# Performance work log

Measured on AMD Instinct MI355X. Metric: run time of the kernel, lower is better.

Reference implementation:

```python
import jax, jax.numpy as jnp
import numpy as np

MU_DT = 0.01
INIT_STD = 0.05

# hidden layers use tanh; last layer is identity (utils.Linear())

def setup_inputs() -> dict:
    key = jax.random.key(0)
    ks = jax.random.split(key, 7)
    B = 512
    nodes = [1024, 4096, 4096, 3072]
    img_batch = jax.random.normal(ks[0], (B, nodes[3]), dtype=jnp.float32)
    mu0 = INIT_STD * jax.random.normal(ks[1], (B, nodes[0]), dtype=jnp.float32)
    mu1 = INIT_STD * jax.random.normal(ks[2], (B, nodes[1]), dtype=jnp.float32)
    mu2 = INIT_STD * jax.random.normal(ks[3], (B, nodes[2]), dtype=jnp.float32)
    W0 = jax.random.normal(ks[4], (nodes[0], nodes[1]), dtype=jnp.float32) / jnp.sqrt(jnp.float32(nodes[0]))
    W1 = jax.random.normal(ks[5], (nodes[1], nodes[2]), dtype=jnp.float32) / jnp.sqrt(jnp.float32(nodes[1]))
    W2 = jax.random.normal(ks[6], (nodes[2], nodes[3]), dtype=jnp.float32) / jnp.sqrt(jnp.float32(nodes[2]))
    return {"img_batch": img_batch, "mu0": mu0, "mu1": mu1, "mu2": mu2,
            "W0": W0, "W1": W1, "W2": W2, "n_iters": 20}


def reference(img_batch, mu0, mu1, mu2, W0, W1, W2, n_iters):
    Ws = (W0, W1, W2)
    L = 3  # n_layers
    acts = (jnp.tanh, jnp.tanh, lambda h: h)
    dacts = (lambda h: 1.0 - jnp.tanh(h) ** 2,
             lambda h: 1.0 - jnp.tanh(h) ** 2,
             lambda h: jnp.ones_like(h))

    def preds_errs(mus):
        # preds[0] = 0, so errs[0] = mus[0]
        hs, errs = [], [mus[0]]
        for l in range(L):
            h = mus[l] @ Ws[l]          # [B, nodes[l+1]]
            hs.append(h)
            errs.append(mus[l + 1] - acts[l](h))
        return hs, errs

    def body(mus, _):
        # prediction pass with current mus (matches stored layer inputs/errs)
        hs, errs = preds_errs(mus)
        new_mus = []
        for l in range(L):
            back = (errs[l + 1] * dacts[l](hs[l])) @ Ws[l].T
            new_mus.append(mus[l] + MU_DT * (back - errs[l]))
        new_mus.append(mus[L])  # target clamped
        return tuple(new_mus), None

    mus = (mu0, mu1, mu2, img_batch)
    mus, _ = jax.lax.scan(body, mus, None, length=n_iters)
    # final prediction/error pass (end of last torch iteration)
    _, errs = preds_errs(mus)
    return jnp.concatenate(errs, axis=1)  # [B, 1024+4096+4096+3072]
```

## Files before the change

### kernel.cpp

```cpp
#include <hip/hip_runtime.h>
#include <hip/hip_bf16.h>
#include <stdint.h>

typedef __hip_bfloat16 bf16_t;
typedef __attribute__((ext_vector_type(8))) short bf16x8;
typedef __attribute__((ext_vector_type(4))) float f32x4;

#define MU_DT 0.01f

__device__ inline void gload_lds16(const void* g, void* lds) {
  __builtin_amdgcn_global_load_lds((const __attribute__((address_space(1))) void*)g,
                                   (__attribute__((address_space(3))) void*)lds, 16, 0, 0);
}

struct GemmLayer {
  const bf16_t* A;
  const bf16_t* Bt;
  const float*  X;
  const float*  E;
  float*        O1;
  bf16_t*       O2;
  int K, N, ostride, mode;
};

struct GemmArgs {
  GemmLayer L[3];
  int start1, start2;
  int tn0, tn1, tn2;
};

__global__ __launch_bounds__(512) void gemm_merged(GemmArgs args) {
  __shared__ __align__(16) bf16_t As[2 * 64 * 64];
  __shared__ __align__(16) bf16_t Bs[2 * 128 * 64];

  const int bid = blockIdx.x;
  int l, local, tilesN;
  if (bid >= args.start2)      { l = 2; local = bid - args.start2; tilesN = args.tn2; }
  else if (bid >= args.start1) { l = 1; local = bid - args.start1; tilesN = args.tn1; }
  else                         { l = 0; local = bid;               tilesN = args.tn0; }
  const GemmLayer Lr = args.L[l];
  const int tm = local / tilesN;
  const int tn = local % tilesN;
  const int K = Lr.K;
  const int rowBase = tm * 64;
  const int colBase = tn * 128;

  const int tid  = threadIdx.x;
  const int lane = tid & 63;
  const int wv   = tid >> 6;
  const int wrM  = wv >> 2;
  const int wcN  = wv & 3;
  const int lo   = lane & 15, hi = lane >> 4;

  f32x4 acc[2][2];
#pragma unroll
  for (int m = 0; m < 2; ++m)
#pragma unroll
    for (int n = 0; n < 2; ++n)
      acc[m][n] = f32x4{0.f, 0.f, 0.f, 0.f};

  char* AsB = (char*)As;
  char* BsB = (char*)Bs;

  const bf16_t* pA0;
  const bf16_t* pB[2];
  {
    const int c = tid;
    const int r = c >> 3, sw = (c & 7) ^ (r & 7);
    pA0 = Lr.A + (size_t)(rowBase + r) * K + sw * 8;
  }
#pragma unroll
  for (int j = 0; j < 2; ++j) {
    const int c = j * 512 + tid;
    const int r = c >> 3, sw = (c & 7) ^ (r & 7);
    pB[j] = Lr.Bt + (size_t)(colBase + r) * K + sw * 8;
  }

  int aoff[2][2], boff[2][2];
#pragma unroll
  for (int m = 0; m < 2; ++m) {
    const int row = wrM * 32 + m * 16 + lo;
#pragma unroll
    for (int kk = 0; kk < 2; ++kk)
      aoff[m][kk] = row * 128 + (((kk * 4 + hi) ^ (row & 7)) << 4);
  }
#pragma unroll
  for (int n = 0; n < 2; ++n) {
    const int row = wcN * 32 + n * 16 + lo;
#pragma unroll
    for (int kk = 0; kk < 2; ++kk)
      boff[n][kk] = row * 128 + (((kk * 4 + hi) ^ (row & 7)) << 4);
  }

  const int waveB = wv * 1024;
  const int nkt = K >> 6;

  gload_lds16(pA0,   AsB + waveB);
  gload_lds16(pB[0], BsB + waveB);
  gload_lds16(pB[1], BsB + 8192 + waveB);
  __syncthreads();

  int cur = 0;
  for (int kt = 0; kt < nkt; ++kt) {
    const int curA = cur * 8192, curB = cur * 16384;
    if (kt + 1 < nkt) {
      const int ke = (kt + 1) * 64;
      gload_lds16(pA0 + ke,   AsB + (curA ^ 8192) + waveB);
      gload_lds16(pB[0] + ke, BsB + (curB ^ 16384) + waveB);
      gload_lds16(pB[1] + ke, BsB + (curB ^ 16384) + 8192 + waveB);
    }

    bf16x8 a[2][2], b[2][2];
#pragma unroll
    for (int m = 0; m < 2; ++m)
#pragma unroll
      for (int kk = 0; kk < 2; ++kk)
        a[m][kk] = *(const bf16x8*)(AsB + curA + aoff[m][kk]);
#pragma unroll
    for (int n = 0; n < 2; ++n)
#pragma unroll
      for (int kk = 0; kk < 2; ++kk)
        b[n][kk] = *(const bf16x8*)(BsB + curB + boff[n][kk]);

#pragma unroll
    for (int kk = 0; kk < 2; ++kk)
#pragma unroll
      for (int m = 0; m < 2; ++m)
#pragma unroll
        for (int n = 0; n < 2; ++n)
          acc[m][n] = __builtin_amdgcn_mfma_f32_16x16x32_bf16(a[m][kk], b[n][kk], acc[m][n], 0, 0, 0);

    if (kt + 1 < nkt) {
      __syncthreads();
      cur ^= 1;
    }
  }

  const int N = Lr.N;
#pragma unroll
  for (int m = 0; m < 2; ++m) {
#pragma unroll
    for (int n = 0; n < 2; ++n) {
#pragma unroll
      for (int r = 0; r < 4; ++r) {
        const int row = rowBase + wrM * 32 + m * 16 + hi * 4 + r;
        const int col = colBase + wcN * 32 + n * 16 + lo;
        const float v = acc[m][n][r];
        const size_t iN = (size_t)row * N + col;
        const size_t iO = (size_t)row * Lr.ostride + col;
        if (Lr.mode == 0) {
          const float mu = Lr.X[iN];
          const float t  = tanhf(v);
          const float e  = mu - t;
          Lr.O1[iO] = e;
          Lr.O2[iN] = __float2bfloat16(e * (1.0f - t * t));
        } else if (Lr.mode == 1) {
          const float e = Lr.X[iN] - v;
          Lr.O1[iO] = e;
          Lr.O2[iN] = __float2bfloat16(e);
        } else if (Lr.mode == 2) {
          const float mu = Lr.X[iN];
          const float nv = mu + MU_DT * (v - mu);
          Lr.O1[iN] = nv;
          Lr.O2[iN] = __float2bfloat16(nv);
        } else {
          const float mu = Lr.X[iN];
          const float e  = Lr.E[iN];
          const float nv = mu + MU_DT * (v - e);
          Lr.O1[iN] = nv;
          Lr.O2[iN] = __float2bfloat16(nv);
        }
      }
    }
  }
}

__global__ void prep_weight(const float* __restrict__ W, bf16_t* __restrict__ Wb,
                            bf16_t* __restrict__ WTb, int R, int C) {
  __shared__ bf16_t t[64][65];
  const int tx = threadIdx.x, ty = threadIdx.y;
  const int c0 = blockIdx.x * 64, r0 = blockIdx.y * 64;
  for (int rr = ty; rr < 64; rr += 4) {
    const float v = W[(size_t)(r0 + rr) * C + c0 + tx];
    const bf16_t b = __float2bfloat16(v);
    Wb[(size_t)(r0 + rr) * C + c0 + tx] = b;
    t[rr][tx] = b;
  }
  __syncthreads();
  for (int rr = ty; rr < 64; rr += 4) {
    WTb[(size_t)(c0 + rr) * R + r0 + tx] = t[tx][rr];
  }
}

__global__ void copy_cast(const float* __restrict__ in, float* __restrict__ of,
                          bf16_t* __restrict__ ob, int n) {
  const int i = blockIdx.x * blockDim.x + threadIdx.x;
  if (i < n) {
    const float v = in[i];
    of[i] = v;
    ob[i] = __float2bfloat16(v);
  }
}

__global__ void copy_e0(const float* __restrict__ mu0, float* __restrict__ out) {
  const int i = blockIdx.x * blockDim.x + threadIdx.x;
  if (i < 512 * 1024) {
    const int b = i >> 10, j = i & 1023;
    out[(size_t)b * 12288 + j] = mu0[i];
  }
}

extern "C" void kernel_launch(void* const* d_in, const int* in_sizes, int n_in,
                              void* d_out, int out_size, void* d_ws, size_t ws_size,
                              hipStream_t stream) {
  const float* img  = (const float*)d_in[0];
  const float* mu0i = (const float*)d_in[1];
  const float* mu1i = (const float*)d_in[2];
  const float* mu2i = (const float*)d_in[3];
  const float* W0   = (const float*)d_in[4];
  const float* W1   = (const float*)d_in[5];
  const float* W2   = (const float*)d_in[6];
  float* out = (float*)d_out;
  const int n_iters = 20;

  char* p = (char*)d_ws;
  auto alloc = [&](size_t bytes) -> char* {
    char* r = p;
    p += (bytes + 255) & ~(size_t)255;
    return r;
  };
  bf16_t* Wb0 = (bf16_t*)alloc((size_t)1024 * 4096 * 2);
  bf16_t* Wb1 = (bf16_t*)alloc((size_t)4096 * 4096 * 2);
  bf16_t* Wb2 = (bf16_t*)alloc((size_t)4096 * 3072 * 2);
  bf16_t* WT0 = (bf16_t*)alloc((size_t)4096 * 1024 * 2);
  bf16_t* WT1 = (bf16_t*)alloc((size_t)4096 * 4096 * 2);
  bf16_t* WT2 = (bf16_t*)alloc((size_t)3072 * 4096 * 2);
  float*  mu0 = (float*)alloc((size_t)512 * 1024 * 4);
  float*  mu1 = (float*)alloc((size_t)512 * 4096 * 4);
  float*  mu2 = (float*)alloc((size_t)512 * 4096 * 4);
  bf16_t* mb0 = (bf16_t*)alloc((size_t)512 * 1024 * 2);
  bf16_t* mb1 = (bf16_t*)alloc((size_t)512 * 4096 * 2);
  bf16_t* mb2 = (bf16_t*)alloc((size_t)512 * 4096 * 2);
  float*  e1  = (float*)alloc((size_t)512 * 4096 * 4);
  float*  e2  = (float*)alloc((size_t)512 * 4096 * 4);
  float*  e3  = (float*)alloc((size_t)512 * 3072 * 4);
  bf16_t* G0  = (bf16_t*)alloc((size_t)512 * 4096 * 2);
  bf16_t* G1  = (bf16_t*)alloc((size_t)512 * 4096 * 2);
  bf16_t* G2  = (bf16_t*)alloc((size_t)512 * 3072 * 2);
  (void)ws_size;

  dim3 tb(64, 4);
  prep_weight<<<dim3(4096 / 64, 1024 / 64), tb, 0, stream>>>(W0, Wb0, WT0, 1024, 4096);
  prep_weight<<<dim3(4096 / 64, 4096 / 64), tb, 0, stream>>>(W1, Wb1, WT1, 4096, 4096);
  prep_weight<<<dim3(3072 / 64, 4096 / 64), tb, 0, stream>>>(W2, Wb2, WT2, 4096, 3072);
  copy_cast<<<(512 * 1024 + 255) / 256, 256, 0, stream>>>(mu0i, mu0, mb0, 512 * 1024);
  copy_cast<<<(512 * 4096 + 255) / 256, 256, 0, stream>>>(mu1i, mu1, mb1, 512 * 4096);
  copy_cast<<<(512 * 4096 + 255) / 256, 256, 0, stream>>>(mu2i, mu2, mb2, 512 * 4096);

  GemmArgs fa;
  fa.L[0] = { mb0, WT0, mu1, nullptr, e1, G0, 1024, 4096, 4096, 0 };
  fa.L[1] = { mb1, WT1, mu2, nullptr, e2, G1, 4096, 4096, 4096, 0 };
  fa.L[2] = { mb2, WT2, img, nullptr, e3, G2, 4096, 3072, 3072, 1 };
  fa.tn0 = 32; fa.tn1 = 32; fa.tn2 = 24;
  fa.start1 = 8 * 32;
  fa.start2 = fa.start1 + 8 * 32;
  const int fwdBlocks = fa.start2 + 8 * 24;

  GemmArgs faF = fa;
  faF.L[0].O1 = out + 1024; faF.L[0].ostride = 12288;
  faF.L[1].O1 = out + 5120; faF.L[1].ostride = 12288;
  faF.L[2].O1 = out + 9216; faF.L[2].ostride = 12288;

  GemmArgs ba;
  ba.L[0] = { G0, Wb0, mu0, nullptr, mu0, mb0, 4096, 1024, 1024, 2 };
  ba.L[1] = { G1, Wb1, mu1, e1,      mu1, mb1, 4096, 4096, 4096, 3 };
  ba.L[2] = { G2, Wb2, mu2, e2,      mu2, mb2, 3072, 4096, 4096, 3 };
  ba.tn0 = 8; ba.tn1 = 32; ba.tn2 = 32;
  ba.start1 = 8 * 8;
  ba.start2 = ba.start1 + 8 * 32;
  const int bwdBlocks = ba.start2 + 8 * 32;

  for (int it = 0; it < n_iters; ++it) {
    gemm_merged<<<fwdBlocks, 512, 0, stream>>>(fa);
    gemm_merged<<<bwdBlocks, 512, 0, stream>>>(ba);
  }
  gemm_merged<<<fwdBlocks, 512, 0, stream>>>(faF);
  copy_e0<<<(512 * 1024 + 255) / 256, 256, 0, stream>>>(mu0, out);
}
```

Before: 2.543 ms.

## Enlarge GEMM tile to 128x128 and reorder blocks to schedule long-K work first

Doubles the M dimension of each block's tile from 64 to 128 rows, so every wave computes a 64x32 sub-tile with twice the MFMAs per LDS load of B. The A staging buffer grows to match, and the LDS double-buffer offset is now a byte toggle. Block-to-layer mapping is replaced by a segment table, so larger-K layers are dispatched first and a layer can be split across segments. The goal is more operand reuse and fewer blocks, at the cost of more registers and LDS per block and coarser load balance with fewer blocks than before.

```diff
diff --git a/kernel.cpp b/kernel.cpp
--- a/kernel.cpp
+++ b/kernel.cpp
@@ -23,26 +23,30 @@
   int K, N, ostride, mode;
 };
 
+struct Seg { int start; int layer; int tnBase; int tilesN; };
+
 struct GemmArgs {
   GemmLayer L[3];
-  int start1, start2;
-  int tn0, tn1, tn2;
+  Seg seg[4];
 };
 
 __global__ __launch_bounds__(512) void gemm_merged(GemmArgs args) {
-  __shared__ __align__(16) bf16_t As[2 * 64 * 64];
+  __shared__ __align__(16) bf16_t As[2 * 128 * 64];
   __shared__ __align__(16) bf16_t Bs[2 * 128 * 64];
 
   const int bid = blockIdx.x;
-  int l, local, tilesN;
-  if (bid >= args.start2)      { l = 2; local = bid - args.start2; tilesN = args.tn2; }
-  else if (bid >= args.start1) { l = 1; local = bid - args.start1; tilesN = args.tn1; }
-  else                         { l = 0; local = bid;               tilesN = args.tn0; }
-  const GemmLayer Lr = args.L[l];
-  const int tm = local / tilesN;
-  const int tn = local % tilesN;
+  int s;
+  if (bid >= args.seg[3].start)      s = 3;
+  else if (bid >= args.seg[2].start) s = 2;
+  else if (bid >= args.seg[1].start) s = 1;
+  else                               s = 0;
+  const Seg sg = args.seg[s];
+  const GemmLayer Lr = args.L[sg.layer];
+  const int local = bid - sg.start;
+  const int tm = local / sg.tilesN;
+  const int tn = sg.tnBase + local % sg.tilesN;
   const int K = Lr.K;
-  const int rowBase = tm * 64;
+  const int rowBase = tm * 128;
   const int colBase = tn * 128;
 
   const int tid  = threadIdx.x;
@@ -52,9 +56,9 @@
   const int wcN  = wv & 3;
   const int lo   = lane & 15, hi = lane >> 4;
 
-  f32x4 acc[2][2];
-#pragma unroll
-  for (int m = 0; m < 2; ++m)
+  f32x4 acc[4][2];
+#pragma unroll
+  for (int m = 0; m < 4; ++m)
 #pragma unroll
     for (int n = 0; n < 2; ++n)
       acc[m][n] = f32x4{0.f, 0.f, 0.f, 0.f};
@@ -62,24 +66,20 @@
   char* AsB = (char*)As;
   char* BsB = (char*)Bs;
 
-  const bf16_t* pA0;
+  const bf16_t* pA[2];
   const bf16_t* pB[2];
-  {
-    const int c = tid;
-    const int r = c >> 3, sw = (c & 7) ^ (r & 7);
-    pA0 = Lr.A + (size_t)(rowBase + r) * K + sw * 8;
-  }
 #pragma unroll
   for (int j = 0; j < 2; ++j) {
     const int c = j * 512 + tid;
     const int r = c >> 3, sw = (c & 7) ^ (r & 7);
+    pA[j] = Lr.A  + (size_t)(rowBase + r) * K + sw * 8;
     pB[j] = Lr.Bt + (size_t)(colBase + r) * K + sw * 8;
   }
 
-  int aoff[2][2], boff[2][2];
-#pragma unroll
-  for (int m = 0; m < 2; ++m) {
-    const int row = wrM * 32 + m * 16 + lo;
+  int aoff[4][2], boff[2][2];
+#pragma unroll
+  for (int m = 0; m < 4; ++m) {
+    const int row = wrM * 64 + m * 16 + lo;
 #pragma unroll
     for (int kk = 0; kk < 2; ++kk)
       aoff[m][kk] = row * 128 + (((kk * 4 + hi) ^ (row & 7)) << 4);
@@ -95,55 +95,59 @@
   const int waveB = wv * 1024;
   const int nkt = K >> 6;
 
-  gload_lds16(pA0,   AsB + waveB);
-  gload_lds16(pB[0], BsB + waveB);
-  gload_lds16(pB[1], BsB + 8192 + waveB);
+#pragma unroll
+  for (int j = 0; j < 2; ++j) {
+    gload_lds16(pA[j], AsB + j * 8192 + waveB);
+    gload_lds16(pB[j], BsB + j * 8192 + waveB);
+  }
   __syncthreads();
 
   int cur = 0;
   for (int kt = 0; kt < nkt; ++kt) {
-    const int curA = cur * 8192, curB = cur * 16384;
     if (kt + 1 < nkt) {
       const int ke = (kt + 1) * 64;
-      gload_lds16(pA0 + ke,   AsB + (curA ^ 8192) + waveB);
-      gload_lds16(pB[0] + ke, BsB + (curB ^ 16384) + waveB);
-      gload_lds16(pB[1] + ke, BsB + (curB ^ 16384) + 8192 + waveB);
+      const int nxt = cur ^ 16384;
+#pragma unroll
+      for (int j = 0; j < 2; ++j) {
+        gload_lds16(pA[j] + ke, AsB + nxt + j * 8192 + waveB);
+        gload_lds16(pB[j] + ke, BsB + nxt + j * 8192 + waveB);
+      }
     }
 
-    bf16x8 a[2][2], b[2][2];
-#pragma unroll
-    for (int m = 0; m < 2; ++m)
+    bf16x8 a[4][2], b[2][2];
+#pragma unroll
+    for (int m = 0; m < 4; ++m)
 #pragma unroll
       for (int kk = 0; kk < 2; ++kk)
-        a[m][kk] = *(const bf16x8*)(AsB + curA + aoff[m][kk]);
+        a[m][kk] = *(const bf16x8*)(AsB + cur + aoff[m][kk]);
 #pragma unroll
     for (int n = 0; n < 2; ++n)
 #pragma unroll
       for (int kk = 0; kk < 2; ++kk)
-        b[n][kk] = *(const bf16x8*)(BsB + curB + boff[n][kk]);
+        b[n][kk] = *(const bf16x8*)(BsB + cur + boff[n][kk]);
 
 #pragma unroll
     for (int kk = 0; kk < 2; ++kk)
 #pragma unroll
-      for (int m = 0; m < 2; ++m)
+      for (int m = 0; m < 4; ++m)
 #pragma unroll
         for (int n = 0; n < 2; ++n)
           acc[m][n] = __builtin_amdgcn_mfma_f32_16x16x32_bf16(a[m][kk], b[n][kk], acc[m][n], 0, 0, 0);
 
     if (kt + 1 < nkt) {
       __syncthreads();
-      cur ^= 1;
+      cur ^= 16384;
     }
   }
 
   const int N = Lr.N;
 #pragma unroll
-  for (int m = 0; m < 2; ++m) {
+  for (int m = 0; m < 4; ++m) {
 #pragma unroll
     for (int n = 0; n < 2; ++n) {
 #pragma unroll
       for (int r = 0; r < 4; ++r) {
-        const int row = rowBase + wrM * 32 + m * 16 + hi * 4 + r;
+        const int row = rowBase + wrM * 64 + m * 16 + hi * 4 + r;
         const int col = colBase + wcN * 32 + n * 16 + lo;
         const float v = acc[m][n][r];
         const size_t iN = (size_t)row * N + col;
@@ -261,10 +265,11 @@
   fa.L[0] = { mb0, WT0, mu1, nullptr, e1, G0, 1024, 4096, 4096, 0 };
   fa.L[1] = { mb1, WT1, mu2, nullptr, e2, G1, 4096, 4096, 4096, 0 };
   fa.L[2] = { mb2, WT2, img, nullptr, e3, G2, 4096, 3072, 3072, 1 };
-  fa.tn0 = 32; fa.tn1 = 32; fa.tn2 = 24;
-  fa.start1 = 8 * 32;
-  fa.start2 = fa.start1 + 8 * 32;
-  const int fwdBlocks = fa.start2 + 8 * 24;
+  fa.seg[0] = { 0,   1, 0, 32 };
+  fa.seg[1] = { 128, 2, 0, 24 };
+  fa.seg[2] = { 224, 0, 0, 32 };
+  fa.seg[3] = { 1 << 30, 0, 0, 1 };
+  const int fwdBlocks = 352;
 
   GemmArgs faF = fa;
   faF.L[0].O1 = out + 1024; faF.L[0].ostride = 12288;
@@ -275,10 +280,11 @@
   ba.L[0] = { G0, Wb0, mu0, nullptr, mu0, mb0, 4096, 1024, 1024, 2 };
   ba.L[1] = { G1, Wb1, mu1, e1,      mu1, mb1, 4096, 4096, 4096, 3 };
   ba.L[2] = { G2, Wb2, mu2, e2,      mu2, mb2, 3072, 4096, 4096, 3 };
-  ba.tn0 = 8; ba.tn1 = 32; ba.tn2 = 32;
-  ba.start1 = 8 * 8;
-  ba.start2 = ba.start1 + 8 * 32;
-  const int bwdBlocks = ba.start2 + 8 * 32;
+  ba.seg[0] = { 0,   2, 0, 8 };
+  ba.seg[1] = { 32,  1, 0, 32 };
+  ba.seg[2] = { 160, 0, 0, 8 };
+  ba.seg[3] = { 192, 2, 8, 24 };
+  const int bwdBlocks = 288;
 
   for (int it = 0; it < n_iters; ++it) {
     gemm_merged<<<fwdBlocks, 512, 0, stream>>>(fa);
```

New measurement: 3.158 ms. +24.2%, slower.
